# Optimization experiments

Hardware: AMD Instinct MI355X
Metric: run time of the kernel (lower is better)

The kernel has to match this reference:

```python
import jax, jax.numpy as jnp
import numpy as np

D_MODEL = 512
NUM_HEADS = 8
D_K = D_MODEL // NUM_HEADS
SCALE = float(np.sqrt(D_K))


def setup_inputs() -> dict:
    key = jax.random.key(0)
    ks = jax.random.split(key, 11)
    B, S, D = 2, 4096, D_MODEL
    std = 1.0 / np.sqrt(D)
    return {
        "query": jax.random.normal(ks[0], (B, S, D), jnp.float32),
        "key": jax.random.normal(ks[1], (B, S, D), jnp.float32),
        "value": jax.random.normal(ks[2], (B, S, D), jnp.float32),
        "w_q": jax.random.normal(ks[3], (D, D), jnp.float32) * std,
        "b_q": jax.random.normal(ks[4], (D,), jnp.float32) * std,
        "w_k": jax.random.normal(ks[5], (D, D), jnp.float32) * std,
        "b_k": jax.random.normal(ks[6], (D,), jnp.float32) * std,
        "w_v": jax.random.normal(ks[7], (D, D), jnp.float32) * std,
        "b_v": jax.random.normal(ks[8], (D,), jnp.float32) * std,
        "w_o": jax.random.normal(ks[9], (D, D), jnp.float32) * std,
        "b_o": jax.random.normal(ks[10], (D,), jnp.float32) * std,
    }


def reference(query, key, value, w_q, b_q, w_k, b_k, w_v, b_v, w_o, b_o):
    B, S, D = query.shape
    H, Dk = NUM_HEADS, D_K
    # Linear projections (torch Linear: x @ W^T + b), split into heads -> [B,H,S,Dk]
    Q = (query @ w_q.T + b_q).reshape(B, S, H, Dk).transpose(0, 2, 1, 3)
    K = (key @ w_k.T + b_k).reshape(B, S, H, Dk).transpose(0, 2, 1, 3)
    V = (value @ w_v.T + b_v).reshape(B, S, H, Dk).transpose(0, 2, 1, 3)
    # [B,H,S,S] attention scores — intentionally materialized like the original
    scores = jnp.einsum("bhqd,bhkd->bhqk", Q, K) / SCALE
    attn = jax.nn.softmax(scores, axis=-1)  # dropout rate 0 in eval baseline
    attended = jnp.einsum("bhqk,bhkd->bhqd", attn, V)
    attended = attended.transpose(0, 2, 1, 3).reshape(B, S, D)
    return attended @ w_o.T + b_o
```

## Files before the change

kernel.cpp:

```cpp
#include <hip/hip_runtime.h>
#include <math.h>

#define D_MODEL 512
#define NHEADS 8
#define DK 64
#define BATCH 2
#define SEQ 4096
#define NIT 32
#define ATTN_SCALE 0.18033688011112043f

typedef _Float16 half8 __attribute__((ext_vector_type(8)));
typedef _Float16 half4 __attribute__((ext_vector_type(4)));
typedef __fp16 pkhalf2 __attribute__((ext_vector_type(2)));
typedef float f32x4 __attribute__((ext_vector_type(4)));

union Pk8 { _Float16 h[8]; uint4 u; };
union Pk4 { _Float16 h[4]; uint2 u; };
union Pkz { pkhalf2 h2[2]; uint2 u; };
union Un4 { uint2 u; _Float16 h[4]; };
union H4  { pkhalf2 p2[2]; half4 h4; };

#if __has_builtin(__builtin_amdgcn_exp2f)
#define EXP2F __builtin_amdgcn_exp2f
#else
#define EXP2F exp2f
#endif

#define MFMA16(a, b, c)   __builtin_amdgcn_mfma_f32_16x16x32_f16((a), (b), (c), 0, 0, 0)
#define MFMA16K16(a, b, c) __builtin_amdgcn_mfma_f32_16x16x16f16((a), (b), (c), 0, 0, 0)

__device__ __forceinline__ void gload_lds16(const _Float16* g, _Float16* l) {
    __builtin_amdgcn_global_load_lds(
        (const __attribute__((address_space(1))) void*)g,
        (__attribute__((address_space(3))) void*)l, 16, 0, 0);
}

__device__ __forceinline__ f32x4 splat4(float v) {
    return (f32x4){v, v, v, v};
}

#define ABLK 4096
#define WBLK 256
__global__ __launch_bounds__(256)
void prep(const float* __restrict__ aq, const float* __restrict__ ak,
          const float* __restrict__ av,
          const float* __restrict__ wq, const float* __restrict__ wk,
          const float* __restrict__ wv, const float* __restrict__ wo,
          _Float16* __restrict__ dq, _Float16* __restrict__ dk,
          _Float16* __restrict__ dv,
          _Float16* __restrict__ hq, _Float16* __restrict__ hk,
          _Float16* __restrict__ hv, _Float16* __restrict__ ho) {
    int gid = blockIdx.x;
    const float* src;
    _Float16* hi;
    if (gid < 3 * ABLK) {
        const int w = gid / ABLK;
        gid -= w * ABLK;
        src = w == 0 ? aq : (w == 1 ? ak : av);
        hi  = w == 0 ? dq : (w == 1 ? dk : dv);
    } else {
        int g = gid - 3 * ABLK;
        const int w = g / WBLK;
        gid = g - w * WBLK;
        src = w == 0 ? wq : (w == 1 ? wk : (w == 2 ? wv : wo));
        hi  = w == 0 ? hq : (w == 1 ? hk : (w == 2 ? hv : ho));
    }
    const int i = (gid * 256 + threadIdx.x) * 4;
    float4 v = *(const float4*)(src + i);
    Pkz h;
    h.h2[0] = __builtin_amdgcn_cvt_pkrtz(v.x, v.y);
    h.h2[1] = __builtin_amdgcn_cvt_pkrtz(v.z, v.w);
    *(uint2*)(hi + i) = h.u;
}

__global__ __launch_bounds__(256)
void gemm_qkv(const _Float16* __restrict__ Aq, const _Float16* __restrict__ Ak,
              const _Float16* __restrict__ Av,
              const _Float16* __restrict__ Whq, const _Float16* __restrict__ Whk,
              const _Float16* __restrict__ Whv,
              const float* __restrict__ bq, const float* __restrict__ bk,
              const float* __restrict__ bv,
              _Float16* __restrict__ Qf, _Float16* __restrict__ Kf,
              _Float16* __restrict__ Vtf) {
    const int z = blockIdx.z;
    const _Float16* A    = z == 0 ? Aq  : (z == 1 ? Ak  : Av);
    const _Float16* Wh   = z == 0 ? Whq : (z == 1 ? Whk : Whv);
    const float*    bias = z == 0 ? bq  : (z == 1 ? bk  : bv);

    __shared__ __align__(16) _Float16 sA[2][128 * 64];
    __shared__ __align__(16) _Float16 sW[2][128 * 64];

    const int t    = threadIdx.x;
    const int lane = t & 63, wave = t >> 6;
    const int col  = lane & 15, quad = lane >> 4;
    const int wm   = (wave & 1) * 64, wn = (wave >> 1) * 64;
    const int m0   = blockIdx.y * 128, n0 = blockIdx.x * 128;

    const int subrow = lane >> 3;
    const int schunk = ((lane & 7) ^ subrow) * 8;

    #define STAGE_AW(K0, BUF)                                                        \
        do {                                                                          \
            _Pragma("unroll")                                                         \
            for (int j = 0; j < 4; ++j) {                                             \
                const int rw = wave * 32 + j * 8;                                     \
                gload_lds16(A  + (size_t)(m0 + rw + subrow) * 512 + (K0) + schunk,    \
                            &sA[BUF][rw * 64]);                                       \
                gload_lds16(Wh + (size_t)(n0 + rw + subrow) * 512 + (K0) + schunk,    \
                            &sW[BUF][rw * 64]);                                       \
            }                                                                         \
        } while (0)

    f32x4 acc[4][4] = {};

    STAGE_AW(0, 0);
    for (int ck = 0; ck < 8; ++ck) {
        const int cur = ck & 1;
        __syncthreads();
        if (ck + 1 < 8) STAGE_AW((ck + 1) * 64, cur ^ 1);

        #pragma unroll
        for (int kc = 0; kc < 2; ++kc) {
            const int pos = ((kc * 4 + quad) ^ (col & 7)) * 8;
            half8 af[4], wf[4];
            #pragma unroll
            for (int mt = 0; mt < 4; ++mt)
                af[mt] = *(const half8*)&sA[cur][(wm + mt * 16 + col) * 64 + pos];
            #pragma unroll
            for (int nt = 0; nt < 4; ++nt)
                wf[nt] = *(const half8*)&sW[cur][(wn + nt * 16 + col) * 64 + pos];
            #pragma unroll
            for (int mt = 0; mt < 4; ++mt)
                #pragma unroll
                for (int nt = 0; nt < 4; ++nt)
                    acc[mt][nt] = MFMA16(af[mt], wf[nt], acc[mt][nt]);
        }
    }

    float bv4[4];
    #pragma unroll
    for (int nt = 0; nt < 4; ++nt) bv4[nt] = bias[n0 + wn + nt * 16 + col];

    if (z < 2) {
        _Float16* Out = z == 0 ? Qf : Kf;
        const float alpha = z == 0 ? ATTN_SCALE : 1.0f;
        #pragma unroll
        for (int mt = 0; mt < 4; ++mt) {
            const int m = m0 + wm + mt * 16 + quad * 4;
            #pragma unroll
            for (int nt = 0; nt < 4; ++nt) {
                const int n = n0 + wn + nt * 16 + col;
                #pragma unroll
                for (int r = 0; r < 4; ++r)
                    Out[(size_t)(m + r) * 512 + n] = (_Float16)((acc[mt][nt][r] + bv4[nt]) * alpha);
            }
        }
    } else {
        #pragma unroll
        for (int mt = 0; mt < 4; ++mt) {
            const int m = m0 + wm + mt * 16 + quad * 4;
            const int b = m >> 12, s = m & (SEQ - 1);
            #pragma unroll
            for (int nt = 0; nt < 4; ++nt) {
                const int n = n0 + wn + nt * 16 + col;
                const int hh = n >> 6, d = n & (DK - 1);
                Pk4 p;
                #pragma unroll
                for (int r = 0; r < 4; ++r)
                    p.h[r] = (_Float16)(acc[mt][nt][r] + bv4[nt]);
                *(uint2*)&Vtf[((size_t)((b * NHEADS + hh) * DK + d)) * SEQ + s] = p.u;
            }
        }
    }
}

__global__ __launch_bounds__(256)
void attn_mfma(const _Float16* __restrict__ Qf, const _Float16* __restrict__ Kf,
               const _Float16* __restrict__ Vtf,
               _Float16* __restrict__ Op0, _Float16* __restrict__ Op1,
               float2* __restrict__ Ml) {
    __shared__ __align__(16) _Float16 sK[2][64 * 64];
    __shared__ __align__(16) _Float16 sV[2][64 * 64];

    const int t    = threadIdx.x;
    const int lane = t & 63;
    const int wave = t >> 6;
    const int col  = lane & 15;
    const int quad = lane >> 4;

    const int strm = blockIdx.x;
    const int h  = strm & (NHEADS - 1);
    const int z  = strm >> 3;
    const int b  = z >> 1;
    const int sp = z & 1;
    const int q0 = blockIdx.y * 128;
    const int kBase = sp * (SEQ / 2);

    const size_t rowBase = (size_t)b * SEQ;
    const size_t vBase   = ((size_t)(b * NHEADS + h)) * DK * SEQ;

    const int subrow = lane >> 3;
    const int schunk = ((lane & 7) ^ subrow) * 8;
    const _Float16* kP[2];
    const _Float16* vP[2];
    #pragma unroll
    for (int j = 0; j < 2; ++j) {
        const int rw = wave * 16 + j * 8;
        kP[j] = Kf + (rowBase + kBase + rw + subrow) * 512 + h * 64 + schunk;
        vP[j] = Vtf + vBase + (size_t)(rw + subrow) * SEQ + kBase + schunk;
        gload_lds16(kP[j], &sK[0][rw * 64]);
        gload_lds16(vP[j], &sV[0][rw * 64]);
        kP[j] += 64 * 512;
        vP[j] += 64;
    }

    half8 qf[2][2];
    #pragma unroll
    for (int nt = 0; nt < 2; ++nt)
        #pragma unroll
        for (int kc = 0; kc < 2; ++kc)
            qf[nt][kc] = *(const half8*)(Qf +
                (rowBase + q0 + wave * 32 + nt * 16 + col) * 512 +
                h * 64 + (kc * 4 + quad) * 8);

    const int cmsk = col & 7;
    const int vsub = ((quad & 1) << 2) + ((quad >> 1) << 3 >> 0);

    float m_r[2] = { 0.0f, 0.0f };
    float l_r[2] = { 0.0f, 0.0f };
    f32x4 of[4][2] = {};

    for (int itp = 0; itp < NIT; itp += 2) {
        #pragma unroll
        for (int cur = 0; cur < 2; ++cur) {
            const int it = itp + cur;
            __syncthreads();
            if (it + 1 < NIT) {
                #pragma unroll
                for (int j = 0; j < 2; ++j) {
                    const int rw = wave * 16 + j * 8;
                    gload_lds16(kP[j], &sK[cur ^ 1][rw * 64]);
                    gload_lds16(vP[j], &sV[cur ^ 1][rw * 64]);
                    kP[j] += 64 * 512;
                    vP[j] += 64;
                }
            }

            f32x4 sf[4][2];
            #pragma unroll
            for (int kt = 0; kt < 4; ++kt) {
                sf[kt][0] = splat4(-m_r[0]);
                sf[kt][1] = splat4(-m_r[1]);
            }
            __builtin_amdgcn_s_setprio(1);
            #pragma unroll
            for (int kc = 0; kc < 2; ++kc) {
                const int pos = ((kc * 4 + quad) ^ cmsk) * 8;
                #pragma unroll
                for (int kt = 0; kt < 4; ++kt) {
                    half8 kf = *(const half8*)&sK[cur][(kt * 16 + col) * 64 + pos];
                    sf[kt][0] = MFMA16(kf, qf[0][kc], sf[kt][0]);
                    sf[kt][1] = MFMA16(kf, qf[1][kc], sf[kt][1]);
                }
            }
            __builtin_amdgcn_s_setprio(0);

            if (it == 0) {
                #pragma unroll
                for (int nt = 0; nt < 2; ++nt) {
                    float mx = sf[0][nt][0];
                    #pragma unroll
                    for (int kt = 0; kt < 4; ++kt)
                        #pragma unroll
                        for (int r = 0; r < 4; ++r)
                            mx = fmaxf(mx, sf[kt][nt][r]);
                    mx = fmaxf(mx, __shfl_xor(mx, 16));
                    mx = fmaxf(mx, __shfl_xor(mx, 32));
                    m_r[nt] = mx;
                    #pragma unroll
                    for (int kt = 0; kt < 4; ++kt)
                        #pragma unroll
                        for (int r = 0; r < 4; ++r)
                            sf[kt][nt][r] -= mx;
                }
            }

            float lrs[2] = { 0.0f, 0.0f };
            #pragma unroll
            for (int kt = 0; kt < 4; ++kt) {
                half4 pf[2];
                #pragma unroll
                for (int nt = 0; nt < 2; ++nt) {
                    const float p0 = EXP2F(sf[kt][nt][0]);
                    const float p1 = EXP2F(sf[kt][nt][1]);
                    const float p2 = EXP2F(sf[kt][nt][2]);
                    const float p3 = EXP2F(sf[kt][nt][3]);
                    lrs[nt] += (p0 + p1) + (p2 + p3);
                    H4 u;
                    u.p2[0] = __builtin_amdgcn_cvt_pkrtz(p0, p1);
                    u.p2[1] = __builtin_amdgcn_cvt_pkrtz(p2, p3);
                    pf[nt] = u.h4;
                }
                const int vofs = ((((kt * 2) + (quad >> 1)) ^ cmsk) << 3) +
                                 ((quad & 1) << 2);
                __builtin_amdgcn_s_setprio(1);
                #pragma unroll
                for (int dt = 0; dt < 4; ++dt) {
                    half4 vf = *(const half4*)&sV[cur][(dt * 16 + col) * 64 + vofs];
                    of[dt][0] = MFMA16K16(vf, pf[0], of[dt][0]);
                    of[dt][1] = MFMA16K16(vf, pf[1], of[dt][1]);
                }
                __builtin_amdgcn_s_setprio(0);
            }

            l_r[0] += lrs[0];
            l_r[1] += lrs[1];

            if (__any(fmaxf(lrs[0], lrs[1]) > 1024.0f)) {
                #pragma unroll
                for (int nt = 0; nt < 2; ++nt) {
                    float mx = sf[0][nt][0];
                    #pragma unroll
                    for (int kt = 0; kt < 4; ++kt)
                        #pragma unroll
                        for (int r = 0; r < 4; ++r)
                            mx = fmaxf(mx, sf[kt][nt][r]);
                    mx = fmaxf(mx, __shfl_xor(mx, 16));
                    mx = fmaxf(mx, __shfl_xor(mx, 32));
                    if (mx > 0.0f) {
                        const float al = EXP2F(-mx);
                        l_r[nt] *= al;
                        #pragma unroll
                        for (int dt = 0; dt < 4; ++dt)
                            #pragma unroll
                            for (int r = 0; r < 4; ++r)
                                of[dt][nt][r] *= al;
                        m_r[nt] += mx;
                    }
                }
            }
        }
    }

    _Float16* Opx = sp ? Op1 : Op0;
    #pragma unroll
    for (int nt = 0; nt < 2; ++nt) {
        float l = l_r[nt];
        l += __shfl_xor(l, 16);
        l += __shfl_xor(l, 32);
        const float inv = 1.0f / l;
        const int q = q0 + wave * 32 + nt * 16 + col;
        const size_t R = (size_t)b * SEQ + q;
        #pragma unroll
        for (int dt = 0; dt < 4; ++dt) {
            Pkz z2;
            z2.h2[0] = __builtin_amdgcn_cvt_pkrtz(of[dt][nt][0] * inv, of[dt][nt][1] * inv);
            z2.h2[1] = __builtin_amdgcn_cvt_pkrtz(of[dt][nt][2] * inv, of[dt][nt][3] * inv);
            *(uint2*)(Opx + R * 512 + h * 64 + dt * 16 + quad * 4) = z2.u;
        }
        if (quad == 0)
            Ml[(size_t)(sp * BATCH * SEQ) * NHEADS + R * NHEADS + h] = make_float2(m_r[nt], l);
    }
}

__global__ __launch_bounds__(256)
void attn_merge(const _Float16* __restrict__ Op0, const _Float16* __restrict__ Op1,
                const float2* __restrict__ Ml, _Float16* __restrict__ Oh) {
    const int i4 = (blockIdx.x * 256 + threadIdx.x) * 4;
    const int R = i4 >> 9;
    const int c = i4 & 511;
    const int h = c >> 6;

    const float2 ml1 = Ml[(size_t)R * NHEADS + h];
    const float2 ml2 = Ml[(size_t)(BATCH * SEQ) * NHEADS + (size_t)R * NHEADS + h];
    const float m = fmaxf(ml1.x, ml2.x);
    float w1 = EXP2F(ml1.x - m) * ml1.y;
    float w2 = EXP2F(ml2.x - m) * ml2.y;
    const float inv = 1.0f / (w1 + w2);
    w1 *= inv; w2 *= inv;

    Un4 a, bb;
    a.u  = *(const uint2*)(Op0 + (size_t)R * 512 + c);
    bb.u = *(const uint2*)(Op1 + (size_t)R * 512 + c);

    Pkz hh;
    hh.h2[0] = __builtin_amdgcn_cvt_pkrtz(w1 * (float)a.h[0] + w2 * (float)bb.h[0],
                                          w1 * (float)a.h[1] + w2 * (float)bb.h[1]);
    hh.h2[1] = __builtin_amdgcn_cvt_pkrtz(w1 * (float)a.h[2] + w2 * (float)bb.h[2],
                                          w1 * (float)a.h[3] + w2 * (float)bb.h[3]);
    *(uint2*)(Oh + (size_t)R * 512 + c) = hh.u;
}

__global__ __launch_bounds__(256)
void gemm_out(const _Float16* __restrict__ Ah, const _Float16* __restrict__ Wh,
              const float* __restrict__ bias, float* __restrict__ C) {
    __shared__ __align__(16) _Float16 sAh[2][128 * 64];
    __shared__ __align__(16) _Float16 sWh[2][64 * 64];

    const int t    = threadIdx.x;
    const int lane = t & 63, wave = t >> 6;
    const int col  = lane & 15, quad = lane >> 4;
    const int wm   = (wave & 1) * 64, wn = (wave >> 1) * 32;
    const int m0   = blockIdx.y * 128, n0 = blockIdx.x * 64;

    const int subrow = lane >> 3;
    const int schunk = ((lane & 7) ^ subrow) * 8;

    #define STAGE_OUT(K0, BUF)                                                       \
        do {                                                                          \
            _Pragma("unroll")                                                         \
            for (int j = 0; j < 4; ++j) {                                             \
                const int rw = wave * 32 + j * 8;                                     \
                gload_lds16(Ah + (size_t)(m0 + rw + subrow) * 512 + (K0) + schunk,    \
                            &sAh[BUF][rw * 64]);                                      \
            }                                                                         \
            _Pragma("unroll")                                                         \
            for (int j = 0; j < 2; ++j) {                                             \
                const int rw = wave * 16 + j * 8;                                     \
                gload_lds16(Wh + (size_t)(n0 + rw + subrow) * 512 + (K0) + schunk,    \
                            &sWh[BUF][rw * 64]);                                      \
            }                                                                         \
        } while (0)

    f32x4 acc[4][2] = {};

    STAGE_OUT(0, 0);
    for (int ck = 0; ck < 8; ++ck) {
        const int cur = ck & 1;
        __syncthreads();
        if (ck + 1 < 8) STAGE_OUT((ck + 1) * 64, cur ^ 1);

        #pragma unroll
        for (int kc = 0; kc < 2; ++kc) {
            const int pos = ((kc * 4 + quad) ^ (col & 7)) * 8;
            half8 ahf[4], whf[2];
            #pragma unroll
            for (int mt = 0; mt < 4; ++mt)
                ahf[mt] = *(const half8*)&sAh[cur][(wm + mt * 16 + col) * 64 + pos];
            #pragma unroll
            for (int nt = 0; nt < 2; ++nt)
                whf[nt] = *(const half8*)&sWh[cur][(wn + nt * 16 + col) * 64 + pos];
            #pragma unroll
            for (int mt = 0; mt < 4; ++mt)
                #pragma unroll
                for (int nt = 0; nt < 2; ++nt)
                    acc[mt][nt] = MFMA16(ahf[mt], whf[nt], acc[mt][nt]);
        }
    }

    float bv2[2];
    #pragma unroll
    for (int nt = 0; nt < 2; ++nt) bv2[nt] = bias[n0 + wn + nt * 16 + col];

    #pragma unroll
    for (int mt = 0; mt < 4; ++mt) {
        const int m = m0 + wm + mt * 16 + quad * 4;
        #pragma unroll
        for (int nt = 0; nt < 2; ++nt) {
            const int n = n0 + wn + nt * 16 + col;
            #pragma unroll
            for (int r = 0; r < 4; ++r)
                C[(size_t)(m + r) * 512 + n] = acc[mt][nt][r] + bv2[nt];
        }
    }
}

extern "C" void kernel_launch(void* const* d_in, const int* in_sizes, int n_in,
                              void* d_out, int out_size, void* d_ws, size_t ws_size,
                              hipStream_t stream) {
    const float* query = (const float*)d_in[0];
    const float* key   = (const float*)d_in[1];
    const float* value = (const float*)d_in[2];
    const float* w_q   = (const float*)d_in[3];
    const float* b_q   = (const float*)d_in[4];
    const float* w_k   = (const float*)d_in[5];
    const float* b_k   = (const float*)d_in[6];
    const float* w_v   = (const float*)d_in[7];
    const float* b_v   = (const float*)d_in[8];
    const float* w_o   = (const float*)d_in[9];
    const float* b_o   = (const float*)d_in[10];
    float* out = (float*)d_out;

    const int WN = D_MODEL * D_MODEL;
    const size_t plane = (size_t)BATCH * SEQ * D_MODEL;

    _Float16* base = (_Float16*)d_ws;
    _Float16* Aq16 = base;
    _Float16* Ak16 = Aq16 + plane;
    _Float16* Av16 = Ak16 + plane;
    _Float16* whq  = Av16 + plane;
    _Float16* whk  = whq + WN;
    _Float16* whv  = whk + WN;
    _Float16* who  = whv + WN;
    _Float16* Qf   = who + WN;
    _Float16* Kf   = Qf + plane;
    _Float16* Vtf  = Kf + plane;
    _Float16* Op1  = Vtf + plane;
    float2*   Ml   = (float2*)(Op1 + plane);
    _Float16* Oh   = Aq16;
    _Float16* Op0  = Av16;

    dim3 blk(256);

    hipLaunchKernelGGL(prep, dim3(3 * ABLK + 4 * WBLK), blk, 0, stream,
                       query, key, value, w_q, w_k, w_v, w_o,
                       Aq16, Ak16, Av16, whq, whk, whv, who);

    hipLaunchKernelGGL(gemm_qkv, dim3(D_MODEL / 128, BATCH * SEQ / 128, 3), blk, 0, stream,
                       Aq16, Ak16, Av16,
                       whq, whk, whv,
                       b_q, b_k, b_v, Qf, Kf, Vtf);

    hipLaunchKernelGGL(attn_mfma, dim3(NHEADS * BATCH * 2, SEQ / 128), blk, 0, stream,
                       Qf, Kf, Vtf, Op0, Op1, Ml);

    hipLaunchKernelGGL(attn_merge, dim3(BATCH * SEQ * D_MODEL / 4 / 256), blk, 0, stream,
                       Op0, Op1, Ml, Oh);

    hipLaunchKernelGGL(gemm_out, dim3(D_MODEL / 64, BATCH * SEQ / 128), blk, 0, stream,
                       Oh, who, b_o, out);
}
```

Before: 261.3 us.

## Switch attention kernel to 32x32x16 MFMA with permlane32 swap for P fragments

```diff
diff --git a/kernel.cpp b/kernel.cpp
--- a/kernel.cpp
+++ b/kernel.cpp
@@ -13,12 +13,13 @@
 typedef _Float16 half4 __attribute__((ext_vector_type(4)));
 typedef __fp16 pkhalf2 __attribute__((ext_vector_type(2)));
 typedef float f32x4 __attribute__((ext_vector_type(4)));
+typedef float f32x16 __attribute__((ext_vector_type(16)));
 
 union Pk8 { _Float16 h[8]; uint4 u; };
 union Pk4 { _Float16 h[4]; uint2 u; };
 union Pkz { pkhalf2 h2[2]; uint2 u; };
 union Un4 { uint2 u; _Float16 h[4]; };
-union H4  { pkhalf2 p2[2]; half4 h4; };
+union PFu { unsigned int u[4]; half8 h8; };
 
 #if __has_builtin(__builtin_amdgcn_exp2f)
 #define EXP2F __builtin_amdgcn_exp2f
@@ -26,17 +27,21 @@
 #define EXP2F exp2f
 #endif
 
-#define MFMA16(a, b, c)   __builtin_amdgcn_mfma_f32_16x16x32_f16((a), (b), (c), 0, 0, 0)
-#define MFMA16K16(a, b, c) __builtin_amdgcn_mfma_f32_16x16x16f16((a), (b), (c), 0, 0, 0)
+#define MFMA16(a, b, c) __builtin_amdgcn_mfma_f32_16x16x32_f16((a), (b), (c), 0, 0, 0)
+#define MFMA32(a, b, c) __builtin_amdgcn_mfma_f32_32x32x16_f16((a), (b), (c), 0, 0, 0)
+
+#define PLSWAP(x, y) asm volatile("v_permlane32_swap_b32 %0, %1" : "+v"(x), "+v"(y))
+
+__device__ __forceinline__ unsigned int cvtpk(float a, float b) {
+    union { pkhalf2 h; unsigned int u; } u_;
+    u_.h = __builtin_amdgcn_cvt_pkrtz(a, b);
+    return u_.u;
+}
 
 __device__ __forceinline__ void gload_lds16(const _Float16* g, _Float16* l) {
     __builtin_amdgcn_global_load_lds(
         (const __attribute__((address_space(1))) void*)g,
         (__attribute__((address_space(3))) void*)l, 16, 0, 0);
-}
-
-__device__ __forceinline__ f32x4 splat4(float v) {
-    return (f32x4){v, v, v, v};
 }
 
 #define ABLK 4096
@@ -174,7 +179,7 @@
     }
 }
 
-__global__ __launch_bounds__(256)
+__global__ __launch_bounds__(256, 4)
 void attn_mfma(const _Float16* __restrict__ Qf, const _Float16* __restrict__ Kf,
                const _Float16* __restrict__ Vtf,
                _Float16* __restrict__ Op0, _Float16* __restrict__ Op1,
@@ -185,8 +190,8 @@
     const int t    = threadIdx.x;
     const int lane = t & 63;
     const int wave = t >> 6;
-    const int col  = lane & 15;
-    const int quad = lane >> 4;
+    const int l31  = lane & 31;
+    const int g    = lane >> 5;
 
     const int strm = blockIdx.x;
     const int h  = strm & (NHEADS - 1);
@@ -214,21 +219,17 @@
         vP[j] += 64;
     }
 
-    half8 qf[2][2];
+    half8 qf[4];
     #pragma unroll
-    for (int nt = 0; nt < 2; ++nt)
-        #pragma unroll
-        for (int kc = 0; kc < 2; ++kc)
-            qf[nt][kc] = *(const half8*)(Qf +
-                (rowBase + q0 + wave * 32 + nt * 16 + col) * 512 +
-                h * 64 + (kc * 4 + quad) * 8);
-
-    const int cmsk = col & 7;
-    const int vsub = ((quad & 1) << 2) + ((quad >> 1) << 3 >> 0);
-
-    float m_r[2] = { 0.0f, 0.0f };
-    float l_r[2] = { 0.0f, 0.0f };
-    f32x4 of[4][2] = {};
+    for (int kc = 0; kc < 4; ++kc)
+        qf[kc] = *(const half8*)(Qf + (rowBase + q0 + wave * 32 + l31) * 512 +
+                                 h * 64 + kc * 16 + g * 8);
+
+    const int rs = l31 & 7;
+
+    float m_r = 0.0f;
+    float l_r = 0.0f;
+    f32x16 of[2] = {};
 
     for (int itp = 0; itp < NIT; itp += 2) {
         #pragma unroll
@@ -246,121 +247,113 @@
                 }
             }
 
-            f32x4 sf[4][2];
-            #pragma unroll
-            for (int kt = 0; kt < 4; ++kt) {
-                sf[kt][0] = splat4(-m_r[0]);
-                sf[kt][1] = splat4(-m_r[1]);
-            }
+            const float nm = -m_r;
+            f32x16 nb;
+            #pragma unroll
+            for (int j2 = 0; j2 < 16; ++j2) nb[j2] = nm;
+
+            f32x16 sf0, sf1;
             __builtin_amdgcn_s_setprio(1);
             #pragma unroll
-            for (int kc = 0; kc < 2; ++kc) {
-                const int pos = ((kc * 4 + quad) ^ cmsk) * 8;
-                #pragma unroll
-                for (int kt = 0; kt < 4; ++kt) {
-                    half8 kf = *(const half8*)&sK[cur][(kt * 16 + col) * 64 + pos];
-                    sf[kt][0] = MFMA16(kf, qf[0][kc], sf[kt][0]);
-                    sf[kt][1] = MFMA16(kf, qf[1][kc], sf[kt][1]);
+            for (int kc = 0; kc < 4; ++kc) {
+                const int pos = ((kc * 2 + g) ^ rs) * 8;
+                half8 k0 = *(const half8*)&sK[cur][l31 * 64 + pos];
+                half8 k1 = *(const half8*)&sK[cur][(32 + l31) * 64 + pos];
+                sf0 = MFMA32(k0, qf[kc], kc == 0 ? nb : sf0);
+                sf1 = MFMA32(k1, qf[kc], kc == 0 ? nb : sf1);
+            }
+            __builtin_amdgcn_s_setprio(0);
+
+            if (it == 0) {
+                float mx = sf0[0];
+                #pragma unroll
+                for (int j2 = 1; j2 < 16; ++j2) mx = fmaxf(mx, sf0[j2]);
+                #pragma unroll
+                for (int j2 = 0; j2 < 16; ++j2) mx = fmaxf(mx, sf1[j2]);
+                mx = fmaxf(mx, __shfl_xor(mx, 32));
+                m_r = mx;
+                #pragma unroll
+                for (int j2 = 0; j2 < 16; ++j2) { sf0[j2] -= mx; sf1[j2] -= mx; }
+            }
+
+            float lrs = 0.0f;
+            #pragma unroll
+            for (int j2 = 0; j2 < 16; ++j2) { sf0[j2] = EXP2F(sf0[j2]); lrs += sf0[j2]; }
+            #pragma unroll
+            for (int j2 = 0; j2 < 16; ++j2) { sf1[j2] = EXP2F(sf1[j2]); lrs += sf1[j2]; }
+
+            PFu pf[4];
+            #define MKPF(P, O)                                                   \
+                do {                                                             \
+                    unsigned int x1 = cvtpk(P[0], P[1]),  x2 = cvtpk(P[2], P[3]);\
+                    unsigned int y1 = cvtpk(P[4], P[5]),  y2 = cvtpk(P[6], P[7]);\
+                    PLSWAP(x1, y1); PLSWAP(x2, y2);                              \
+                    pf[O].u[0] = x1; pf[O].u[1] = x2;                            \
+                    pf[O].u[2] = y1; pf[O].u[3] = y2;                            \
+                    unsigned int a1 = cvtpk(P[8], P[9]),  a2 = cvtpk(P[10], P[11]);\
+                    unsigned int b1 = cvtpk(P[12], P[13]), b2 = cvtpk(P[14], P[15]);\
+                    PLSWAP(a1, b1); PLSWAP(a2, b2);                              \
+                    pf[O + 1].u[0] = a1; pf[O + 1].u[1] = a2;                    \
+                    pf[O + 1].u[2] = b1; pf[O + 1].u[3] = b2;                    \
+                } while (0)
+            MKPF(sf0, 0);
+            MKPF(sf1, 2);
+            #undef MKPF
+
+            __builtin_amdgcn_s_setprio(1);
+            #pragma unroll
+            for (int ks = 0; ks < 4; ++ks) {
+                const int pos = ((ks * 2 + g) ^ rs) * 8;
+                half8 v0 = *(const half8*)&sV[cur][l31 * 64 + pos];
+                half8 v1 = *(const half8*)&sV[cur][(32 + l31) * 64 + pos];
+                of[0] = MFMA32(v0, pf[ks].h8, of[0]);
+                of[1] = MFMA32(v1, pf[ks].h8, of[1]);
+            }
+            __builtin_amdgcn_s_setprio(0);
+
+            l_r += lrs;
+
+            if (__any(lrs > 1024.0f)) {
+                float pmax = sf0[0];
+                #pragma unroll
+                for (int j2 = 1; j2 < 16; ++j2) pmax = fmaxf(pmax, sf0[j2]);
+                #pragma unroll
+                for (int j2 = 0; j2 < 16; ++j2) pmax = fmaxf(pmax, sf1[j2]);
+                pmax = fmaxf(pmax, __shfl_xor(pmax, 32));
+                if (pmax > 1.0f) {
+                    const float al = 1.0f / pmax;
+                    l_r *= al;
+                    #pragma unroll
+                    for (int dt = 0; dt < 2; ++dt)
+                        #pragma unroll
+                        for (int j2 = 0; j2 < 16; ++j2)
+                            of[dt][j2] *= al;
+                    m_r += __log2f(pmax);
                 }
             }
-            __builtin_amdgcn_s_setprio(0);
-
-            if (it == 0) {
-                #pragma unroll
-                for (int nt = 0; nt < 2; ++nt) {
-                    float mx = sf[0][nt][0];
-                    #pragma unroll
-                    for (int kt = 0; kt < 4; ++kt)
-                        #pragma unroll
-                        for (int r = 0; r < 4; ++r)
-                            mx = fmaxf(mx, sf[kt][nt][r]);
-                    mx = fmaxf(mx, __shfl_xor(mx, 16));
-                    mx = fmaxf(mx, __shfl_xor(mx, 32));
-                    m_r[nt] = mx;
-                    #pragma unroll
-                    for (int kt = 0; kt < 4; ++kt)
-                        #pragma unroll
-                        for (int r = 0; r < 4; ++r)
-                            sf[kt][nt][r] -= mx;
-                }
-            }
-
-            float lrs[2] = { 0.0f, 0.0f };
-            #pragma unroll
-            for (int kt = 0; kt < 4; ++kt) {
-                half4 pf[2];
-                #pragma unroll
-                for (int nt = 0; nt < 2; ++nt) {
-                    const float p0 = EXP2F(sf[kt][nt][0]);
-                    const float p1 = EXP2F(sf[kt][nt][1]);
-                    const float p2 = EXP2F(sf[kt][nt][2]);
-                    const float p3 = EXP2F(sf[kt][nt][3]);
-                    lrs[nt] += (p0 + p1) + (p2 + p3);
-                    H4 u;
-                    u.p2[0] = __builtin_amdgcn_cvt_pkrtz(p0, p1);
-                    u.p2[1] = __builtin_amdgcn_cvt_pkrtz(p2, p3);
-                    pf[nt] = u.h4;
-                }
-                const int vofs = ((((kt * 2) + (quad >> 1)) ^ cmsk) << 3) +
-                                 ((quad & 1) << 2);
-                __builtin_amdgcn_s_setprio(1);
-                #pragma unroll
-                for (int dt = 0; dt < 4; ++dt) {
-                    half4 vf = *(const half4*)&sV[cur][(dt * 16 + col) * 64 + vofs];
-                    of[dt][0] = MFMA16K16(vf, pf[0], of[dt][0]);
-                    of[dt][1] = MFMA16K16(vf, pf[1], of[dt][1]);
-                }
-                __builtin_amdgcn_s_setprio(0);
-            }
-
-            l_r[0] += lrs[0];
-            l_r[1] += lrs[1];
-
-            if (__any(fmaxf(lrs[0], lrs[1]) > 1024.0f)) {
-                #pragma unroll
-                for (int nt = 0; nt < 2; ++nt) {
-                    float mx = sf[0][nt][0];
-                    #pragma unroll
-                    for (int kt = 0; kt < 4; ++kt)
-                        #pragma unroll
-                        for (int r = 0; r < 4; ++r)
-                            mx = fmaxf(mx, sf[kt][nt][r]);
-                    mx = fmaxf(mx, __shfl_xor(mx, 16));
-                    mx = fmaxf(mx, __shfl_xor(mx, 32));
-                    if (mx > 0.0f) {
-                        const float al = EXP2F(-mx);
-                        l_r[nt] *= al;
-                        #pragma unroll
-                        for (int dt = 0; dt < 4; ++dt)
-                            #pragma unroll
-                            for (int r = 0; r < 4; ++r)
-                                of[dt][nt][r] *= al;
-                        m_r[nt] += mx;
-                    }
-                }
-            }
-        }
-    }
-
+        }
+    }
+
+    float l = l_r + __shfl_xor(l_r, 32);
+    const float inv = 1.0f / l;
+    const int q = q0 + wave * 32 + l31;
+    const size_t R = rowBase + q;
     _Float16* Opx = sp ? Op1 : Op0;
     #pragma unroll
-    for (int nt = 0; nt < 2; ++nt) {
-        float l = l_r[nt];
-        l += __shfl_xor(l, 16);
-        l += __shfl_xor(l, 32);
-        const float inv = 1.0f / l;
-        const int q = q0 + wave * 32 + nt * 16 + col;
-        const size_t R = (size_t)b * SEQ + q;
-        #pragma unroll
-        for (int dt = 0; dt < 4; ++dt) {
+    for (int dt = 0; dt < 2; ++dt) {
+        #pragma unroll
+        for (int m4 = 0; m4 < 4; ++m4) {
+            const int d0 = dt * 32 + 8 * m4 + 4 * g;
             Pkz z2;
-            z2.h2[0] = __builtin_amdgcn_cvt_pkrtz(of[dt][nt][0] * inv, of[dt][nt][1] * inv);
-            z2.h2[1] = __builtin_amdgcn_cvt_pkrtz(of[dt][nt][2] * inv, of[dt][nt][3] * inv);
-            *(uint2*)(Opx + R * 512 + h * 64 + dt * 16 + quad * 4) = z2.u;
-        }
-        if (quad == 0)
-            Ml[(size_t)(sp * BATCH * SEQ) * NHEADS + R * NHEADS + h] = make_float2(m_r[nt], l);
-    }
+            z2.h2[0] = __builtin_amdgcn_cvt_pkrtz(of[dt][4 * m4 + 0] * inv,
+                                                  of[dt][4 * m4 + 1] * inv);
+            z2.h2[1] = __builtin_amdgcn_cvt_pkrtz(of[dt][4 * m4 + 2] * inv,
+                                                  of[dt][4 * m4 + 3] * inv);
+            *(uint2*)(Opx + R * 512 + h * 64 + d0) = z2.u;
+        }
+    }
+    if (lane < 32)
+        Ml[(size_t)(sp * BATCH * SEQ) * NHEADS + R * NHEADS + h] = make_float2(m_r, l);
 }
 
 __global__ __launch_bounds__(256)
```

After: 239.8 us. 8.2% less time.
